# Kernel optimization log

Measured on AMD Instinct MI355X. Metric: run time of the kernel, lower is better.

The kernel has to match this reference:

```python
import jax, jax.numpy as jnp
import numpy as np

NUM_CODES = 512
CODE_DIM = 64
BATCH = 1048576


def setup_inputs() -> dict:
    key = jax.random.key(0)
    k1, k2 = jax.random.split(key)
    z_e = jax.random.normal(k1, (BATCH, CODE_DIM), dtype=jnp.float32)
    bound = 1.0 / np.sqrt(float(CODE_DIM))
    codebook = jax.random.uniform(
        k2, (NUM_CODES, CODE_DIM), dtype=jnp.float32, minval=-bound, maxval=bound
    )
    return {"z_e": z_e, "codebook": codebook}


def reference(z_e, codebook):
    # ||z_e||^2 - 2 z_e . e_j + ||e_j||^2  -> (batch, num_codes)
    distances = (
        jnp.sum(z_e**2, axis=1, keepdims=True)
        - 2.0 * (z_e @ codebook.T)
        + jnp.sum(codebook**2, axis=1)
    )
    indices = jnp.argmin(distances, axis=1)          # (batch,)
    z_q = codebook[indices]                           # gather (batch, code_dim)
    # straight-through estimator
    z_q_st = z_e + jax.lax.stop_gradient(z_q - z_e)
    commitment_loss = jnp.mean((jax.lax.stop_gradient(z_e) - z_q) ** 2)
    return (z_q_st, indices, commitment_loss)
```

## Files before the change

### kernel.cpp

```cpp
#include <hip/hip_runtime.h>
#include <stdint.h>


#define DIM 64
#define NCODE 512
#define RPB 128
#define MARGIN 2e-3f
#define ZEXB 8
#define WS_NEED (NCODE * DIM * 2 * sizeof(unsigned short) + NCODE * sizeof(float))

typedef __attribute__((ext_vector_type(8))) short short8;
typedef __attribute__((ext_vector_type(4))) float f32x4;
typedef unsigned long long ull;

__device__ __forceinline__ float bf2f(unsigned short u) {
    union { unsigned u; float f; } c; c.u = ((unsigned)u) << 16; return c.f;
}
__device__ __forceinline__ unsigned short f2bf(float f) {
    union { float f; unsigned u; } c; c.f = f;
    unsigned r = c.u + 0x7fffu + ((c.u >> 16) & 1u);
    return (unsigned short)(r >> 16);
}
__device__ __forceinline__ unsigned fkey(float v) {
    union { float f; unsigned u; } c; c.f = v;
    return c.u ^ ((unsigned)((int)c.u >> 31) | 0x80000000u);
}
__device__ __forceinline__ float funkey(unsigned k) {
    unsigned u = (k & 0x80000000u) ? (k ^ 0x80000000u) : ~k;
    union { unsigned u; float f; } c; c.u = u; return c.f;
}

__device__ __forceinline__ float np_sumsq64_sse(const float* x) {
    #pragma clang fp contract(off)
    float T[4];
    #pragma unroll
    for (int l = 0; l < 4; ++l) {
        float A[8];
        #pragma unroll
        for (int j = 0; j < 8; ++j) {
            float u = x[4 * j + l];
            float v = x[32 + 4 * j + l];
            A[j] = u * u + v * v;
        }
        T[l] = ((A[0] + A[1]) + (A[2] + A[3])) + ((A[4] + A[5]) + (A[6] + A[7]));
    }
    return (T[0] + T[1]) + (T[2] + T[3]);
}

__global__ void vq_zero_loss(float* __restrict__ out, long long lidx) {
    if (threadIdx.x == 0) out[lidx] = 0.f;
}

__global__ __launch_bounds__(NCODE) void vq_prep(
    const float* __restrict__ cb, unsigned short* __restrict__ ws)
{
    const int code = threadIdx.x;
    unsigned short* cbhi = ws;
    unsigned short* cblo = ws + NCODE * DIM;
    float* ce2g = (float*)(ws + 2 * NCODE * DIM);

    float sp[4];
    #pragma unroll
    for (int cl = 0; cl < 4; ++cl) {
        float s = 0.f;
        #pragma unroll
        for (int ks = 0; ks < 2; ++ks) {
            #pragma unroll
            for (int t = 0; t < 8; ++t) {
                int k = ks * 32 + cl * 8 + t;
                float v = cb[code * DIM + k];
                unsigned short hb = f2bf(v);
                cbhi[code * DIM + k] = hb;
                cblo[code * DIM + k] = f2bf(v - bf2f(hb));
                s = fmaf(v, v, s);
            }
        }
        sp[cl] = s;
    }
    ce2g[code] = (sp[0] + sp[1]) + (sp[2] + sp[3]);
}

template <bool PRE>
__global__ __launch_bounds__(512) void vq_main(
    const float* __restrict__ z, const float* __restrict__ cb,
    float* __restrict__ out, const unsigned short* __restrict__ ws,
    long long batch)
{
    __shared__ __align__(16) unsigned short zhi[RPB * DIM];
    __shared__ __align__(16) unsigned short zlo[RPB * DIM];
    __shared__ float zsq[RPB];
    __shared__ ull arrP[16][8][17];
    __shared__ unsigned arrS[16][8][17];
    __shared__ ull cpack[RPB];
    __shared__ unsigned ck2[RPB];
    __shared__ float wsum[8];
    __shared__ int s_flag[RPB];
    __shared__ int s_nflag;
    __shared__ float s_zex[ZEXB][DIM];
    __shared__ ull s_win[ZEXB];

    const int tid = threadIdx.x, lane = tid & 63, wid = tid >> 6;
    const long long R0 = (long long)blockIdx.x * RPB;
    short8* zhi8 = (short8*)zhi;
    short8* zlo8 = (short8*)zlo;

    if (tid == 0) s_nflag = 0;

    #pragma unroll
    for (int p = 0; p < 2; ++p) {
        int L = p * 512 + tid;
        int row = L >> 3, c = L & 7;
        const float4* g = (const float4*)(z + (R0 + row) * DIM + c * 8);
        float4 f0 = g[0], f1 = g[1];
        float v[8] = {f0.x, f0.y, f0.z, f0.w, f1.x, f1.y, f1.z, f1.w};
        short8 h, l;
        float s = 0.f;
        #pragma unroll
        for (int t = 0; t < 8; ++t) {
            unsigned short hb = f2bf(v[t]);
            h[t] = (short)hb;
            l[t] = (short)f2bf(v[t] - bf2f(hb));
            s = fmaf(v[t], v[t], s);
        }
        s += __shfl_xor(s, 1);
        s += __shfl_xor(s, 2);
        s += __shfl_xor(s, 4);
        if ((tid & 7) == 0) zsq[row] = s;
        int slot = row * 8 + (c ^ (row & 7));
        zhi8[slot] = h;
        zlo8[slot] = l;
    }

    short8 bhi[4][2], blo[4][2];
    float ce2[4];
    if constexpr (PRE) {
        const unsigned short* cbhi = ws;
        const unsigned short* cblo = ws + NCODE * DIM;
        const float* ce2g = (const float*)(ws + 2 * NCODE * DIM);
        #pragma unroll
        for (int ct = 0; ct < 4; ++ct) {
            int code = wid * 64 + ct * 16 + (lane & 15);
            #pragma unroll
            for (int ks = 0; ks < 2; ++ks) {
                int k = ks * 32 + (lane >> 4) * 8;
                bhi[ct][ks] = *(const short8*)(cbhi + code * DIM + k);
                blo[ct][ks] = *(const short8*)(cblo + code * DIM + k);
            }
            ce2[ct] = ce2g[code];
        }
    } else {
        #pragma unroll
        for (int ct = 0; ct < 4; ++ct) {
            int code = wid * 64 + ct * 16 + (lane & 15);
            float s = 0.f;
            #pragma unroll
            for (int ks = 0; ks < 2; ++ks) {
                int k = ks * 32 + (lane >> 4) * 8;
                const float4* g = (const float4*)(cb + code * DIM + k);
                float4 f0 = g[0], f1 = g[1];
                float v[8] = {f0.x, f0.y, f0.z, f0.w, f1.x, f1.y, f1.z, f1.w};
                short8 h, l;
                #pragma unroll
                for (int t = 0; t < 8; ++t) {
                    unsigned short hb = f2bf(v[t]);
                    h[t] = (short)hb;
                    l[t] = (short)f2bf(v[t] - bf2f(hb));
                    s = fmaf(v[t], v[t], s);
                }
                bhi[ct][ks] = h;
                blo[ct][ks] = l;
            }
            s += __shfl_xor(s, 16);
            s += __shfl_xor(s, 32);
            ce2[ct] = s;
        }
    }

    __syncthreads();

    for (int rt = 0; rt < 8; ++rt) {
        int arow = rt * 16 + (lane & 15);
        int swz = arow & 7;
        int c0 = (lane >> 4) ^ swz, c1 = (4 + (lane >> 4)) ^ swz;
        short8 ah0 = zhi8[arow * 8 + c0], ah1 = zhi8[arow * 8 + c1];
        short8 al0 = zlo8[arow * 8 + c0], al1 = zlo8[arow * 8 + c1];

        f32x4 accs[4];
        #pragma unroll
        for (int ct = 0; ct < 4; ++ct) {
            f32x4 a = {0.f, 0.f, 0.f, 0.f};
            a = __builtin_amdgcn_mfma_f32_16x16x32_bf16(ah0, bhi[ct][0], a, 0, 0, 0);
            a = __builtin_amdgcn_mfma_f32_16x16x32_bf16(ah1, bhi[ct][1], a, 0, 0, 0);
            a = __builtin_amdgcn_mfma_f32_16x16x32_bf16(ah0, blo[ct][0], a, 0, 0, 0);
            a = __builtin_amdgcn_mfma_f32_16x16x32_bf16(ah1, blo[ct][1], a, 0, 0, 0);
            a = __builtin_amdgcn_mfma_f32_16x16x32_bf16(al0, bhi[ct][0], a, 0, 0, 0);
            a = __builtin_amdgcn_mfma_f32_16x16x32_bf16(al1, bhi[ct][1], a, 0, 0, 0);
            accs[ct] = a;
        }

        #pragma unroll
        for (int r = 0; r < 4; ++r) {
            unsigned bk = 0xFFFFFFFFu, bk2 = 0xFFFFFFFFu, bi = 0;
            #pragma unroll
            for (int ct = 0; ct < 4; ++ct) {
                float v = fmaf(-2.f, accs[ct][r], ce2[ct]);
                unsigned k = fkey(v);
                unsigned idx = (unsigned)(wid * 64 + ct * 16 + (lane & 15));
                if (k < bk)       { bk2 = bk; bk = k; bi = idx; }
                else if (k < bk2) { bk2 = k; }
            }
            int rl = (lane >> 4) * 4 + r;
            arrP[rl][wid][lane & 15] = ((ull)bk << 32) | bi;
            arrS[rl][wid][lane & 15] = bk2;
        }
        __syncthreads();

        if (tid < 128) {
            int rl = tid >> 3, w = tid & 7;
            ull b = arrP[rl][w][0];
            unsigned k2 = arrS[rl][w][0];
            #pragma unroll
            for (int l = 1; l < 16; ++l) {
                ull ob = arrP[rl][w][l];
                unsigned ok2 = arrS[rl][w][l];
                unsigned k1o = (unsigned)(ob >> 32);
                unsigned k1s = (unsigned)(b >> 32);
                k2 = min(min(k2, ok2), max(k1o, k1s));
                if (ob < b) b = ob;
            }
            #pragma unroll
            for (int m = 1; m <= 4; m <<= 1) {
                ull ob = __shfl_xor(b, m);
                unsigned ok2 = __shfl_xor(k2, m);
                unsigned k1o = (unsigned)(ob >> 32);
                unsigned k1s = (unsigned)(b >> 32);
                k2 = min(min(k2, ok2), max(k1o, k1s));
                if (ob < b) b = ob;
            }
            if (w == 0) {
                cpack[rt * 16 + rl] = b;
                ck2[rt * 16 + rl] = k2;
            }
        }
        __syncthreads();
    }

    {
        int row = tid >> 2, j = tid & 3;
        ull best = cpack[row];
        unsigned bk2 = ck2[row];
        unsigned code = (unsigned)best;
        long long grow = R0 + row;

        float4* out4 = (float4*)out;
        const float4* cb4 = (const float4*)cb;
        #pragma unroll
        for (int t = 0; t < 4; ++t)
            out4[grow * 16 + j * 4 + t] = cb4[(long long)code * 16 + j * 4 + t];

        float d = 0.f;
        if (j == 0) {
            out[batch * DIM + grow] = (float)code;
            float v1 = funkey((unsigned)(best >> 32));
            float v2 = funkey(bk2);
            d = zsq[row] + v1;
            if (v2 - v1 < MARGIN) {
                int p = atomicAdd(&s_nflag, 1);
                s_flag[p] = row;
            }
        }
        #pragma unroll
        for (int m = 1; m < 64; m <<= 1) d += __shfl_xor(d, m);
        if (lane == 0) wsum[wid] = d;
    }
    __syncthreads();
    if (tid == 0) {
        float s = 0.f;
        #pragma unroll
        for (int w = 0; w < 8; ++w) s += wsum[w];
        atomicAdd(&out[batch * DIM + batch], s * (1.0f / 67108864.0f));
    }

    int nf = s_nflag;
    if (nf > 0) {
        float ce[64];
        const float4* cb4 = (const float4*)cb;
        #pragma unroll
        for (int q = 0; q < 16; ++q) {
            float4 v = cb4[tid * 16 + q];
            ce[q * 4 + 0] = v.x; ce[q * 4 + 1] = v.y;
            ce[q * 4 + 2] = v.z; ce[q * 4 + 3] = v.w;
        }
        float s2 = np_sumsq64_sse(ce);

        for (int b0 = 0; b0 < nf; b0 += ZEXB) {
            int nb = min(ZEXB, nf - b0);
            if (tid < nb * 64) {
                int i = tid >> 6, l2 = tid & 63;
                s_zex[i][l2] = z[(R0 + s_flag[b0 + i]) * DIM + l2];
            }
            if (tid < ZEXB) s_win[tid] = ~0ull;
            __syncthreads();

            for (int i = 0; i < nb; ++i) {
                float s1 = np_sumsq64_sse(&s_zex[i][0]);
                float m = 0.f;
                #pragma unroll
                for (int k = 0; k < 64; ++k)
                    m = __builtin_fmaf(s_zex[i][k], ce[k], m);
                float dnp;
                {
                    #pragma clang fp contract(off)
                    float tt = s1 - 2.0f * m;
                    dnp = tt + s2;
                }
                ull key = ((ull)fkey(dnp) << 10) | (unsigned)tid;
                #pragma unroll
                for (int mm = 1; mm < 64; mm <<= 1) {
                    ull o = __shfl_xor(key, mm);
                    if (o < key) key = o;
                }
                if (lane == 0) atomicMin(&s_win[i], key);
            }
            __syncthreads();

            for (int i = wid; i < nb; i += 8) {
                unsigned code = (unsigned)(s_win[i] & 0x3FFull);
                int rowb = s_flag[b0 + i];
                long long grow = R0 + rowb;
                out[grow * DIM + lane] = cb[(long long)code * DIM + lane];
                if (lane == 0) out[batch * DIM + grow] = (float)code;
            }
            __syncthreads();
        }
    }
}

extern "C" void kernel_launch(void* const* d_in, const int* in_sizes, int n_in,
                              void* d_out, int out_size, void* d_ws, size_t ws_size,
                              hipStream_t stream)
{
    const float* z  = (const float*)d_in[0];
    const float* cb = (const float*)d_in[1];
    float* out = (float*)d_out;
    unsigned short* ws = (unsigned short*)d_ws;

    long long batch = (long long)in_sizes[0] / DIM;
    int nblocks = (int)(batch / RPB);
    long long lidx = batch * DIM + batch;

    vq_zero_loss<<<1, 64, 0, stream>>>(out, lidx);
    if (d_ws != nullptr && ws_size >= WS_NEED) {
        vq_prep<<<1, NCODE, 0, stream>>>(cb, ws);
        vq_main<true><<<nblocks, 512, 0, stream>>>(z, cb, out, ws, batch);
    } else {
        vq_main<false><<<nblocks, 512, 0, stream>>>(z, cb, out, ws, batch);
    }
}
```

Measured before the change: 690.6 us.

## Make each wave own its rows and stream all codes, removing cross-wave reduction

Each wave now owns 32 rows, with their A fragments held in registers, and loops over all 512 codes, streaming codebook fragments from global/L2 each iteration. Before, each wave held 64 codes and every row tile went through an LDS cross-wave argmin with two barriers. The change removes the per-tile LDS reduction and barriers, doubles rows per block to 256, and reduces argmin within the wave using shuffles. In exchange every wave re-reads the full codebook per block, which adds L2 traffic, and LDS use grows with the doubled row tile, which may reduce occupancy.

```diff
diff --git a/kernel.cpp b/kernel.cpp
--- a/kernel.cpp
+++ b/kernel.cpp
@@ -4,7 +4,8 @@
 
 #define DIM 64
 #define NCODE 512
-#define RPB 128
+#define RPB 256
+#define TPW 2
 #define MARGIN 2e-3f
 #define ZEXB 8
 #define WS_NEED (NCODE * DIM * 2 * sizeof(unsigned short) + NCODE * sizeof(float))
@@ -89,8 +90,6 @@
     __shared__ __align__(16) unsigned short zhi[RPB * DIM];
     __shared__ __align__(16) unsigned short zlo[RPB * DIM];
     __shared__ float zsq[RPB];
-    __shared__ ull arrP[16][8][17];
-    __shared__ unsigned arrS[16][8][17];
     __shared__ ull cpack[RPB];
     __shared__ unsigned ck2[RPB];
     __shared__ float wsum[8];
@@ -100,6 +99,7 @@
     __shared__ ull s_win[ZEXB];
 
     const int tid = threadIdx.x, lane = tid & 63, wid = tid >> 6;
+    const int cl = lane >> 4, l15 = lane & 15;
     const long long R0 = (long long)blockIdx.x * RPB;
     short8* zhi8 = (short8*)zhi;
     short8* zlo8 = (short8*)zlo;
@@ -107,7 +107,7 @@
     if (tid == 0) s_nflag = 0;
 
     #pragma unroll
-    for (int p = 0; p < 2; ++p) {
+    for (int p = 0; p < 4; ++p) {
         int L = p * 512 + tid;
         int row = L >> 3, c = L & 7;
         const float4* g = (const float4*)(z + (R0 + row) * DIM + c * 8);
@@ -130,34 +130,47 @@
         zhi8[slot] = h;
         zlo8[slot] = l;
     }
-
-    short8 bhi[4][2], blo[4][2];
-    float ce2[4];
-    if constexpr (PRE) {
-        const unsigned short* cbhi = ws;
-        const unsigned short* cblo = ws + NCODE * DIM;
-        const float* ce2g = (const float*)(ws + 2 * NCODE * DIM);
-        #pragma unroll
-        for (int ct = 0; ct < 4; ++ct) {
-            int code = wid * 64 + ct * 16 + (lane & 15);
-            #pragma unroll
-            for (int ks = 0; ks < 2; ++ks) {
-                int k = ks * 32 + (lane >> 4) * 8;
-                bhi[ct][ks] = *(const short8*)(cbhi + code * DIM + k);
-                blo[ct][ks] = *(const short8*)(cblo + code * DIM + k);
-            }
-            ce2[ct] = ce2g[code];
-        }
-    } else {
-        #pragma unroll
-        for (int ct = 0; ct < 4; ++ct) {
-            int code = wid * 64 + ct * 16 + (lane & 15);
+    __syncthreads();
+
+    short8 ah0[TPW], ah1[TPW], al0[TPW], al1[TPW];
+    #pragma unroll
+    for (int t = 0; t < TPW; ++t) {
+        int arow = wid * 32 + t * 16 + l15;
+        int swz = arow & 7;
+        int c0 = cl ^ swz, c1 = (4 + cl) ^ swz;
+        ah0[t] = zhi8[arow * 8 + c0];
+        ah1[t] = zhi8[arow * 8 + c1];
+        al0[t] = zlo8[arow * 8 + c0];
+        al1[t] = zlo8[arow * 8 + c1];
+    }
+
+    unsigned bk[TPW][4], bk2[TPW][4], bi[TPW][4];
+    #pragma unroll
+    for (int t = 0; t < TPW; ++t)
+        #pragma unroll
+        for (int r = 0; r < 4; ++r) { bk[t][r] = 0xFFFFFFFFu; bk2[t][r] = 0xFFFFFFFFu; bi[t][r] = 0; }
+
+    const unsigned short* cbhi = ws;
+    const unsigned short* cblo = ws + NCODE * DIM;
+    const float* ce2g = (const float*)(ws + 2 * NCODE * DIM);
+
+    #pragma unroll 2
+    for (int g = 0; g < 32; ++g) {
+        const int code = g * 16 + l15;
+        short8 bh0, bh1, bl0, bl1;
+        float ce2;
+        if constexpr (PRE) {
+            bh0 = *(const short8*)(cbhi + code * DIM + cl * 8);
+            bh1 = *(const short8*)(cbhi + code * DIM + 32 + cl * 8);
+            bl0 = *(const short8*)(cblo + code * DIM + cl * 8);
+            bl1 = *(const short8*)(cblo + code * DIM + 32 + cl * 8);
+            ce2 = ce2g[code];
+        } else {
             float s = 0.f;
             #pragma unroll
             for (int ks = 0; ks < 2; ++ks) {
-                int k = ks * 32 + (lane >> 4) * 8;
-                const float4* g = (const float4*)(cb + code * DIM + k);
-                float4 f0 = g[0], f1 = g[1];
+                const float4* gp = (const float4*)(cb + code * DIM + ks * 32 + cl * 8);
+                float4 f0 = gp[0], f1 = gp[1];
                 float v[8] = {f0.x, f0.y, f0.z, f0.w, f1.x, f1.y, f1.z, f1.w};
                 short8 h, l;
                 #pragma unroll
@@ -167,102 +180,75 @@
                     l[t] = (short)f2bf(v[t] - bf2f(hb));
                     s = fmaf(v[t], v[t], s);
                 }
-                bhi[ct][ks] = h;
-                blo[ct][ks] = l;
+                if (ks == 0) { bh0 = h; bl0 = l; } else { bh1 = h; bl1 = l; }
             }
             s += __shfl_xor(s, 16);
             s += __shfl_xor(s, 32);
-            ce2[ct] = s;
-        }
-    }
-
+            ce2 = s;
+        }
+
+        #pragma unroll
+        for (int t = 0; t < TPW; ++t) {
+            f32x4 a = {0.f, 0.f, 0.f, 0.f};
+            a = __builtin_amdgcn_mfma_f32_16x16x32_bf16(ah0[t], bh0, a, 0, 0, 0);
+            a = __builtin_amdgcn_mfma_f32_16x16x32_bf16(ah1[t], bh1, a, 0, 0, 0);
+            a = __builtin_amdgcn_mfma_f32_16x16x32_bf16(ah0[t], bl0, a, 0, 0, 0);
+            a = __builtin_amdgcn_mfma_f32_16x16x32_bf16(ah1[t], bl1, a, 0, 0, 0);
+            a = __builtin_amdgcn_mfma_f32_16x16x32_bf16(al0[t], bh0, a, 0, 0, 0);
+            a = __builtin_amdgcn_mfma_f32_16x16x32_bf16(al1[t], bh1, a, 0, 0, 0);
+            #pragma unroll
+            for (int r = 0; r < 4; ++r) {
+                float v = fmaf(-2.f, a[r], ce2);
+                unsigned k = fkey(v);
+                unsigned idx = (unsigned)code;
+                if (k < bk[t][r])       { bk2[t][r] = bk[t][r]; bk[t][r] = k; bi[t][r] = idx; }
+                else if (k < bk2[t][r]) { bk2[t][r] = k; }
+            }
+        }
+    }
+
+    #pragma unroll
+    for (int t = 0; t < TPW; ++t) {
+        #pragma unroll
+        for (int r = 0; r < 4; ++r) {
+            ull best = ((ull)bk[t][r] << 32) | bi[t][r];
+            unsigned b2 = bk2[t][r];
+            #pragma unroll
+            for (int m = 1; m <= 8; m <<= 1) {
+                ull ob = __shfl_xor(best, m);
+                unsigned ok2 = __shfl_xor(b2, m);
+                unsigned k1o = (unsigned)(ob >> 32);
+                unsigned k1s = (unsigned)(best >> 32);
+                b2 = min(min(b2, ok2), max(k1o, k1s));
+                if (ob < best) best = ob;
+            }
+            if (l15 == 0) {
+                int row = wid * 32 + t * 16 + cl * 4 + r;
+                cpack[row] = best;
+                ck2[row] = b2;
+            }
+        }
+    }
     __syncthreads();
 
-    for (int rt = 0; rt < 8; ++rt) {
-        int arow = rt * 16 + (lane & 15);
-        int swz = arow & 7;
-        int c0 = (lane >> 4) ^ swz, c1 = (4 + (lane >> 4)) ^ swz;
-        short8 ah0 = zhi8[arow * 8 + c0], ah1 = zhi8[arow * 8 + c1];
-        short8 al0 = zlo8[arow * 8 + c0], al1 = zlo8[arow * 8 + c1];
-
-        f32x4 accs[4];
-        #pragma unroll
-        for (int ct = 0; ct < 4; ++ct) {
-            f32x4 a = {0.f, 0.f, 0.f, 0.f};
-            a = __builtin_amdgcn_mfma_f32_16x16x32_bf16(ah0, bhi[ct][0], a, 0, 0, 0);
-            a = __builtin_amdgcn_mfma_f32_16x16x32_bf16(ah1, bhi[ct][1], a, 0, 0, 0);
-            a = __builtin_amdgcn_mfma_f32_16x16x32_bf16(ah0, blo[ct][0], a, 0, 0, 0);
-            a = __builtin_amdgcn_mfma_f32_16x16x32_bf16(ah1, blo[ct][1], a, 0, 0, 0);
-            a = __builtin_amdgcn_mfma_f32_16x16x32_bf16(al0, bhi[ct][0], a, 0, 0, 0);
-            a = __builtin_amdgcn_mfma_f32_16x16x32_bf16(al1, bhi[ct][1], a, 0, 0, 0);
-            accs[ct] = a;
-        }
-
-        #pragma unroll
-        for (int r = 0; r < 4; ++r) {
-            unsigned bk = 0xFFFFFFFFu, bk2 = 0xFFFFFFFFu, bi = 0;
-            #pragma unroll
-            for (int ct = 0; ct < 4; ++ct) {
-                float v = fmaf(-2.f, accs[ct][r], ce2[ct]);
-                unsigned k = fkey(v);
-                unsigned idx = (unsigned)(wid * 64 + ct * 16 + (lane & 15));
-                if (k < bk)       { bk2 = bk; bk = k; bi = idx; }
-                else if (k < bk2) { bk2 = k; }
-            }
-            int rl = (lane >> 4) * 4 + r;
-            arrP[rl][wid][lane & 15] = ((ull)bk << 32) | bi;
-            arrS[rl][wid][lane & 15] = bk2;
-        }
-        __syncthreads();
-
-        if (tid < 128) {
-            int rl = tid >> 3, w = tid & 7;
-            ull b = arrP[rl][w][0];
-            unsigned k2 = arrS[rl][w][0];
-            #pragma unroll
-            for (int l = 1; l < 16; ++l) {
-                ull ob = arrP[rl][w][l];
-                unsigned ok2 = arrS[rl][w][l];
-                unsigned k1o = (unsigned)(ob >> 32);
-                unsigned k1s = (unsigned)(b >> 32);
-                k2 = min(min(k2, ok2), max(k1o, k1s));
-                if (ob < b) b = ob;
-            }
-            #pragma unroll
-            for (int m = 1; m <= 4; m <<= 1) {
-                ull ob = __shfl_xor(b, m);
-                unsigned ok2 = __shfl_xor(k2, m);
-                unsigned k1o = (unsigned)(ob >> 32);
-                unsigned k1s = (unsigned)(b >> 32);
-                k2 = min(min(k2, ok2), max(k1o, k1s));
-                if (ob < b) b = ob;
-            }
-            if (w == 0) {
-                cpack[rt * 16 + rl] = b;
-                ck2[rt * 16 + rl] = k2;
-            }
-        }
-        __syncthreads();
-    }
-
     {
-        int row = tid >> 2, j = tid & 3;
+        int row = tid >> 1, j = tid & 1;
         ull best = cpack[row];
-        unsigned bk2 = ck2[row];
+        unsigned bk2v = ck2[row];
         unsigned code = (unsigned)best;
         long long grow = R0 + row;
 
         float4* out4 = (float4*)out;
         const float4* cb4 = (const float4*)cb;
         #pragma unroll
-        for (int t = 0; t < 4; ++t)
-            out4[grow * 16 + j * 4 + t] = cb4[(long long)code * 16 + j * 4 + t];
+        for (int t = 0; t < 8; ++t)
+            out4[grow * 16 + j * 8 + t] = cb4[(long long)code * 16 + j * 8 + t];
 
         float d = 0.f;
         if (j == 0) {
             out[batch * DIM + grow] = (float)code;
             float v1 = funkey((unsigned)(best >> 32));
-            float v2 = funkey(bk2);
+            float v2 = funkey(bk2v);
             d = zsq[row] + v1;
             if (v2 - v1 < MARGIN) {
                 int p = atomicAdd(&s_nflag, 1);
```

New measurement: 818.7 us. 18.6% more time.
